# Kernel optimization log

Hardware: AMD Instinct MI355X
Metric: run time of the kernel (lower is better)

## Reference

```python
import jax, jax.numpy as jnp
import numpy as np
import math

B, S, D, H = 2, 2048, 1024, 16
DK = D // H


def setup_inputs() -> dict:
    key = jax.random.key(0)
    ks = jax.random.split(key, 12)
    std = 1.0 / math.sqrt(D)
    inp = {
        "q": jax.random.normal(ks[0], (B, S, D), jnp.float32),
        "k": jax.random.normal(ks[1], (B, S, D), jnp.float32),
        "v": jax.random.normal(ks[2], (B, S, D), jnp.float32),
        # causal mask, broadcast over batch and heads
        "mask": jnp.tril(jnp.ones((S, S), jnp.int32))[None, None, :, :],
        "wq": jax.random.normal(ks[3], (D, D), jnp.float32) * std,
        "bq": jax.random.normal(ks[4], (D,), jnp.float32) * std,
        "wk": jax.random.normal(ks[5], (D, D), jnp.float32) * std,
        "bk": jax.random.normal(ks[6], (D,), jnp.float32) * std,
        "wv": jax.random.normal(ks[7], (D, D), jnp.float32) * std,
        "bv": jax.random.normal(ks[8], (D,), jnp.float32) * std,
        "wo": jax.random.normal(ks[9], (D, D), jnp.float32) * std,
        "bo": jax.random.normal(ks[10], (D,), jnp.float32) * std,
    }
    return inp


def _split_heads(x):
    # [B,S,D] -> [B,H,S,DK]
    b, s, _ = x.shape
    return x.reshape(b, s, H, DK).transpose(0, 2, 1, 3)


def reference(q, k, v, mask, wq, bq, wk, bk, wv, bv, wo, bo):
    # nn.Linear: y = x @ W^T + b
    query = _split_heads(q @ wq.T + bq)
    key_h = _split_heads(k @ wk.T + bk)
    value = _split_heads(v @ wv.T + bv)

    scale = 1.0 / math.sqrt(DK)
    scores = jnp.einsum("bhqd,bhkd->bhqk", query, key_h) * scale  # [B,H,S,S]
    scores = jnp.where(mask == 0, jnp.float32(-1e9), scores)
    attn = jax.nn.softmax(scores, axis=-1)  # dropout p=0.0 -> identity

    x = jnp.einsum("bhqk,bhkd->bhqd", attn, value)  # [B,H,S,DK]
    x = x.transpose(0, 2, 1, 3).reshape(q.shape[0], -1, H * DK)  # [B,S,D]
    return x @ wo.T + bo
```

## Files before the change

### kernel.cpp

```cpp
#include <hip/hip_runtime.h>

#define B_SZ    2
#define S_LEN   2048
#define D_MODEL 1024
#define H_NUM   16
#define DK_H    64
#define M_ROWS  (B_SZ * S_LEN)

typedef __attribute__((ext_vector_type(8))) short  short8;
typedef __attribute__((ext_vector_type(4))) short  short4v;
typedef __attribute__((ext_vector_type(4))) float  floatx4;

__device__ __forceinline__ short f2b(float f) {
    union { float f; unsigned u; } x; x.f = f;
    unsigned u = x.u + 0x7fffu + ((x.u >> 16) & 1u);
    return (short)(u >> 16);
}

typedef __attribute__((address_space(1))) const unsigned int gu32;
typedef __attribute__((address_space(3))) unsigned int       lu32;
__device__ __forceinline__ void gload_lds16(const short* g, short* l) {
    __builtin_amdgcn_global_load_lds((gu32*)g, (lu32*)l, 16, 0, 0);
}

#define QSCALE 0.18033688011112042f
#define SM_SHIFT 12.0f

__global__ void cvt_all_kernel(const float* __restrict__ xq, const float* __restrict__ xk,
                               const float* __restrict__ xv, const float* __restrict__ wq,
                               const float* __restrict__ wk, const float* __restrict__ wv,
                               const float* __restrict__ wo,
                               short* __restrict__ oxq, short* __restrict__ oxk,
                               short* __restrict__ oxv, short* __restrict__ owq,
                               short* __restrict__ owk, short* __restrict__ owv,
                               short* __restrict__ owo)
{
    const int y = blockIdx.y;
    const float* in;
    short* out;
    switch (y) {
        case 0: in = xq; out = oxq; break;
        case 1: in = xk; out = oxk; break;
        case 2: in = xv; out = oxv; break;
        case 3: in = wq; out = owq; break;
        case 4: in = wk; out = owk; break;
        case 5: in = wv; out = owv; break;
        default: in = wo; out = owo; break;
    }
    if (y < 3) {
        int base = blockIdx.x * 1024 + threadIdx.x * 4;
        for (int p = 0; p < 4; ++p) {
            int i = base + p * 1048576;
            float4 v = *(const float4*)(in + i);
            short4v r;
            r[0] = f2b(v.x); r[1] = f2b(v.y); r[2] = f2b(v.z); r[3] = f2b(v.w);
            *(short4v*)(out + i) = r;
        }
    } else {
        int f = blockIdx.x * 256 + (int)threadIdx.x;
        if (blockIdx.x < 512) {
            int n4 = f >> 11, rem = f & 2047;
            int k8 = rem >> 4, nl = rem & 15;
            const float* src = in + (size_t)(n4 * 16 + nl) * D_MODEL + k8 * 8;
            float4 v0 = *(const float4*)(src);
            float4 v1 = *(const float4*)(src + 4);
            short8 r;
            r[0] = f2b(v0.x); r[1] = f2b(v0.y); r[2] = f2b(v0.z); r[3] = f2b(v0.w);
            r[4] = f2b(v1.x); r[5] = f2b(v1.y); r[6] = f2b(v1.z); r[7] = f2b(v1.w);
            *(short8*)(out + (size_t)f * 8) = r;
        }
    }
}

__global__ __launch_bounds__(256, 2)
void gemm_qkv_kernel(const short* __restrict__ xq, const short* __restrict__ xk,
                     const short* __restrict__ xv,
                     const short* __restrict__ wq, const short* __restrict__ wk,
                     const short* __restrict__ wv,
                     const float* __restrict__ bq, const float* __restrict__ bk,
                     const float* __restrict__ bv,
                     short* __restrict__ Qp, short* __restrict__ Kp, short* __restrict__ Vt)
{
    __shared__ short sa[128 * 32];

    const int which = blockIdx.y >> 3;
    const short* A    = (which == 0) ? xq : (which == 1) ? xk : xv;
    const short* W    = (which == 0) ? wq : (which == 1) ? wk : wv;
    const float* bias = (which == 0) ? bq : (which == 1) ? bk : bv;
    const float scale = (which == 0) ? QSCALE : 1.0f;

    const int nb = (blockIdx.y & 7) * 128;
    const int m0 = blockIdx.x * 128;
    const int t = threadIdx.x, wave = t >> 6, lane = t & 63;
    const int quad = lane >> 4, l16 = lane & 15;
    const int wm = (wave & 1) * 64, wn = (wave >> 1) * 64;

    const int r0 = t >> 2, cs = t & 3;
    const int c0 = cs ^ ((r0 >> 1) & 3);
    const short* Ab0 = A + (size_t)(m0 + r0) * D_MODEL + c0 * 8;
    const short* Ab1 = Ab0 + (size_t)64 * D_MODEL;
    short* sa0 = sa + t * 8;  short* sa1 = sa + 2048 + t * 8;

    int a_off[4];
#pragma unroll
    for (int i = 0; i < 4; ++i) {
        int ar = wm + i * 16 + l16;
        a_off[i] = ar * 32 + ((quad ^ ((ar >> 1) & 3)) * 8);
    }

    const short* Wt = W + ((size_t)((nb + wn) >> 4) * 128 + quad) * 128 + l16 * 8;

#define LOADB(dst, k0) do { _Pragma("unroll")                                  \
    for (int nt_ = 0; nt_ < 4; ++nt_)                                          \
        dst[nt_] = *(const short8*)(Wt + nt_ * 16384 + (k0) * 16); } while (0)

    short8 bfA[4], bfB[4];
    LOADB(bfA, 0);

    floatx4 acc[4][4] = {};
#pragma unroll 1
    for (int k0 = 0; k0 < D_MODEL; k0 += 64) {
        __syncthreads();
        gload_lds16(Ab0 + k0, sa0);
        gload_lds16(Ab1 + k0, sa1);
        __syncthreads();
        LOADB(bfB, k0 + 32);
#pragma unroll
        for (int mt = 0; mt < 4; ++mt) {
            short8 af = *(const short8*)(sa + a_off[mt]);
#pragma unroll
            for (int nt = 0; nt < 4; ++nt)
                acc[mt][nt] = __builtin_amdgcn_mfma_f32_16x16x32_bf16(af, bfA[nt], acc[mt][nt], 0, 0, 0);
        }
        __syncthreads();
        gload_lds16(Ab0 + k0 + 32, sa0);
        gload_lds16(Ab1 + k0 + 32, sa1);
        __syncthreads();
        if (k0 + 64 < D_MODEL) LOADB(bfA, k0 + 64);
#pragma unroll
        for (int mt = 0; mt < 4; ++mt) {
            short8 af = *(const short8*)(sa + a_off[mt]);
#pragma unroll
            for (int nt = 0; nt < 4; ++nt)
                acc[mt][nt] = __builtin_amdgcn_mfma_f32_16x16x32_bf16(af, bfB[nt], acc[mt][nt], 0, 0, 0);
        }
    }
#undef LOADB

#pragma unroll
    for (int nt = 0; nt < 4; ++nt) {
        int ncol = nb + wn + nt * 16 + l16;
        int h = ncol >> 6, dk = ncol & 63;
        float bv_ = bias[ncol];
#pragma unroll
        for (int mt = 0; mt < 4; ++mt) {
            int mrow0 = m0 + wm + mt * 16 + quad * 4;
            int bb = mrow0 >> 11, s0 = mrow0 & (S_LEN - 1);
            if (which < 2) {
                short* Out = (which == 0) ? Qp : Kp;
#pragma unroll
                for (int r = 0; r < 4; ++r) {
                    float v = (acc[mt][nt][r] + bv_) * scale;
                    Out[(((size_t)bb * H_NUM + h) * S_LEN + (s0 + r)) * DK_H + dk] = f2b(v);
                }
            } else {
                int Sb = s0 & ~63, sb0_ = s0 & 63;
                size_t rowbase = (((size_t)bb * H_NUM + h) * DK_H + dk) * S_LEN + Sb;
#pragma unroll
                for (int r = 0; r < 4; ++r) {
                    int cc = sb0_ + r;
                    Vt[rowbase + ((cc & 15) * 4 + (cc >> 4))] = f2b(acc[mt][nt][r] + bv_);
                }
            }
        }
    }
}

__global__ __launch_bounds__(512, 4)
void attn_kernel(const short* __restrict__ Qp, const short* __restrict__ Kp,
                 const short* __restrict__ Vt, short* __restrict__ Xa)
{
    __shared__ short kbuf[2][64 * 64];
    __shared__ short vbuf[2][64 * 64];
    __shared__ short pl[8][16 * 72];

    const int lin = (int)(blockIdx.x + 16 * blockIdx.y);
    const int bh = lin & 31;
    const int j8 = (lin >> 5) & 7;
    const int tile = (lin >> 8) ? (15 - j8) : j8;

    const int t = threadIdx.x, wave = t >> 6, lane = t & 63;
    const int quad = lane >> 4, l16 = lane & 15;

    const short* Qb  = Qp + (size_t)bh * S_LEN * DK_H;
    const short* Kb  = Kp + (size_t)bh * S_LEN * DK_H;
    const short* Vtb = Vt + (size_t)bh * DK_H * S_LEN;

    const int q0 = tile * 128 + wave * 16;
    const int my_ktimax = 2 * tile + (wave >> 2);
    const int ktb = 2 * tile + 1;

    const int r0 = t >> 3, cs = t & 7;
    const int c0 = cs ^ (r0 & 7);
    const short* Kg = Kb + r0 * DK_H + c0 * 8;
    const short* Vg = Vtb + (size_t)r0 * S_LEN + c0 * 8;
    short* kl0 = &kbuf[0][t * 8]; short* kl1 = &kbuf[1][t * 8];
    short* vl0 = &vbuf[0][t * 8]; short* vl1 = &vbuf[1][t * 8];

    short8 qf[2];
#pragma unroll
    for (int ks = 0; ks < 2; ++ks)
        qf[ks] = *(const short8*)(Qb + (size_t)(q0 + l16) * DK_H + ks * 32 + quad * 8);

    short8 bl = {};
    if (l16 == 0) {
#pragma unroll
        for (int j = 0; j < 8; ++j) bl[j] = (short)0x3F80;
    }

    int fo[4][2];
#pragma unroll
    for (int nt = 0; nt < 4; ++nt)
#pragma unroll
        for (int ks = 0; ks < 2; ++ks) {
            int row = nt * 16 + l16;
            fo[nt][ks] = row * 64 + (((ks * 4 + quad) ^ (l16 & 7)) * 8);
        }

    floatx4 o[4] = {};
    floatx4 ol = {};
    short* plw = &pl[wave][0];
    const int qg = q0 + quad * 4;

    gload_lds16(Kg, kl0);
    gload_lds16(Vg, vl0);
    __syncthreads();

    for (int kti = 0; kti <= ktb; ++kti) {
        const short* kb = (kti & 1) ? &kbuf[1][0] : &kbuf[0][0];
        const short* vb = (kti & 1) ? &vbuf[1][0] : &vbuf[0][0];
        const int kbase = kti * 64;

        if (kti < ktb) {
            gload_lds16(Kg + (size_t)(kbase + 64) * DK_H, (kti & 1) ? kl0 : kl1);
            gload_lds16(Vg + (kbase + 64),                (kti & 1) ? vl0 : vl1);
        }

        if (kti <= my_ktimax) {
            short8 bkf[4][2];
#pragma unroll
            for (int nt = 0; nt < 4; ++nt)
#pragma unroll
                for (int ks = 0; ks < 2; ++ks)
                    bkf[nt][ks] = *(const short8*)(kb + fo[nt][ks]);

            floatx4 sc[4] = {};
#pragma unroll
            for (int nt = 0; nt < 4; ++nt)
#pragma unroll
                for (int ks = 0; ks < 2; ++ks)
                    sc[nt] = __builtin_amdgcn_mfma_f32_16x16x32_bf16(qf[ks], bkf[nt][ks], sc[nt], 0, 0, 0);

            if (kti == my_ktimax) {
#pragma unroll
                for (int nt = 0; nt < 4; ++nt) {
                    int key = kbase + nt * 16 + l16;
#pragma unroll
                    for (int r = 0; r < 4; ++r)
                        if (key > qg + r) sc[nt][r] = -1e30f;
                }
            }

#pragma unroll
            for (int r = 0; r < 4; ++r) {
                union { float f; unsigned u; } a0, a1, a2, a3;
                a0.f = exp2f(sc[0][r] - SM_SHIFT);
                a1.f = exp2f(sc[1][r] - SM_SHIFT);
                a2.f = exp2f(sc[2][r] - SM_SHIFT);
                a3.f = exp2f(sc[3][r] - SM_SHIFT);
                uint2 d;
                d.x = (a1.u & 0xffff0000u) | (a0.u >> 16);
                d.y = (a3.u & 0xffff0000u) | (a2.u >> 16);
                *(uint2*)(plw + (quad * 4 + r) * 72 + l16 * 4) = d;
            }

            short8 ap0 = *(const short8*)(plw + l16 * 72 + quad * 8);
            short8 ap1 = *(const short8*)(plw + l16 * 72 + 32 + quad * 8);

            short8 bvf[4][2];
#pragma unroll
            for (int nt = 0; nt < 4; ++nt)
#pragma unroll
                for (int ks = 0; ks < 2; ++ks)
                    bvf[nt][ks] = *(const short8*)(vb + fo[nt][ks]);

#pragma unroll
            for (int nt = 0; nt < 4; ++nt) {
                o[nt] = __builtin_amdgcn_mfma_f32_16x16x32_bf16(ap0, bvf[nt][0], o[nt], 0, 0, 0);
                o[nt] = __builtin_amdgcn_mfma_f32_16x16x32_bf16(ap1, bvf[nt][1], o[nt], 0, 0, 0);
            }
            ol = __builtin_amdgcn_mfma_f32_16x16x32_bf16(ap0, bl, ol, 0, 0, 0);
            ol = __builtin_amdgcn_mfma_f32_16x16x32_bf16(ap1, bl, ol, 0, 0, 0);
        }

        __syncthreads();
    }

    const int b_ = bh >> 4, h = bh & 15;
#pragma unroll
    for (int r = 0; r < 4; ++r) {
        float lsum = __shfl(ol[r], (lane & 48));
        float rinv = 1.0f / lsum;
        int srow = qg + r;
#pragma unroll
        for (int nt = 0; nt < 4; ++nt) {
            int col = h * 64 + nt * 16 + l16;
            Xa[((size_t)b_ * S_LEN + srow) * D_MODEL + col] = f2b(o[nt][r] * rinv);
        }
    }
}

__global__ __launch_bounds__(256, 2)
void gemm_out_kernel(const short* __restrict__ A, const short* __restrict__ W,
                     const float* __restrict__ bias, float* __restrict__ out)
{
    __shared__ short sa[2][128 * 64];

    const int nb = blockIdx.y * 64;
    const int m0 = blockIdx.x * 128;
    const int t = threadIdx.x, wave = t >> 6, lane = t & 63;
    const int quad = lane >> 4, l16 = lane & 15;
    const int wm = (wave & 1) * 64, wn = (wave >> 1) * 32;

    const int rs = t >> 3;
    const int cl = (t & 7) ^ (rs & 7);
    const short* Asrc = A + (size_t)(m0 + rs) * D_MODEL + cl * 8;
    short* sd0 = &sa[0][t * 8];
    short* sd1 = &sa[1][t * 8];

#define STAGE_A(dst, k0) do { _Pragma("unroll")                                \
    for (int j_ = 0; j_ < 4; ++j_)                                             \
        gload_lds16(Asrc + (size_t)j_ * 32 * D_MODEL + (k0),                   \
                    (dst) + j_ * 2048); } while (0)

    int a_off[4][2];
#pragma unroll
    for (int i = 0; i < 4; ++i) {
        int ar = wm + i * 16 + l16;
#pragma unroll
        for (int ks = 0; ks < 2; ++ks)
            a_off[i][ks] = ar * 64 + (((ks * 4 + quad) ^ (ar & 7)) * 8);
    }

    const short* Wt = W + ((size_t)((nb + wn) >> 4) * 128 + quad) * 128 + l16 * 8;

#define LOADB2(dst, k0) do { _Pragma("unroll")                                 \
    for (int nt_ = 0; nt_ < 2; ++nt_)                                          \
        dst[nt_] = *(const short8*)(Wt + nt_ * 16384 + (k0) * 16); } while (0)

    short8 bfA[2], bfB[2];
    STAGE_A(sd0, 0);
    LOADB2(bfA, 0);
    __syncthreads();

    floatx4 acc[4][2] = {};
#pragma unroll 1
    for (int k0 = 0; k0 < D_MODEL; k0 += 64) {
        const int p = (k0 >> 6) & 1;
        const short* cur = &sa[p][0];
        if (k0 + 64 < D_MODEL) STAGE_A(p ? sd0 : sd1, k0 + 64);
        LOADB2(bfB, k0 + 32);

        short8 af[4][2];
#pragma unroll
        for (int mt = 0; mt < 4; ++mt) {
            af[mt][0] = *(const short8*)(cur + a_off[mt][0]);
            af[mt][1] = *(const short8*)(cur + a_off[mt][1]);
        }
#pragma unroll
        for (int mt = 0; mt < 4; ++mt)
#pragma unroll
            for (int nt = 0; nt < 2; ++nt)
                acc[mt][nt] = __builtin_amdgcn_mfma_f32_16x16x32_bf16(af[mt][0], bfA[nt], acc[mt][nt], 0, 0, 0);
        if (k0 + 64 < D_MODEL) LOADB2(bfA, k0 + 64);
#pragma unroll
        for (int mt = 0; mt < 4; ++mt)
#pragma unroll
            for (int nt = 0; nt < 2; ++nt)
                acc[mt][nt] = __builtin_amdgcn_mfma_f32_16x16x32_bf16(af[mt][1], bfB[nt], acc[mt][nt], 0, 0, 0);
        __syncthreads();
    }
#undef STAGE_A
#undef LOADB2

#pragma unroll
    for (int nt = 0; nt < 2; ++nt) {
        int ncol = nb + wn + nt * 16 + l16;
        float bv_ = bias[ncol];
#pragma unroll
        for (int mt = 0; mt < 4; ++mt) {
            int mrow0 = m0 + wm + mt * 16 + quad * 4;
#pragma unroll
            for (int r = 0; r < 4; ++r)
                out[(size_t)(mrow0 + r) * D_MODEL + ncol] = acc[mt][nt][r] + bv_;
        }
    }
}

extern "C" void kernel_launch(void* const* d_in, const int* in_sizes, int n_in,
                              void* d_out, int out_size, void* d_ws, size_t ws_size,
                              hipStream_t stream)
{
    (void)in_sizes; (void)n_in; (void)out_size; (void)ws_size;
    const float* q  = (const float*)d_in[0];
    const float* k  = (const float*)d_in[1];
    const float* v  = (const float*)d_in[2];
    const float* wq = (const float*)d_in[4];
    const float* bq = (const float*)d_in[5];
    const float* wk = (const float*)d_in[6];
    const float* bk = (const float*)d_in[7];
    const float* wv = (const float*)d_in[8];
    const float* bv = (const float*)d_in[9];
    const float* wo = (const float*)d_in[10];
    const float* bo = (const float*)d_in[11];
    float* out = (float*)d_out;

    const size_t XE = (size_t)M_ROWS * D_MODEL;
    const size_t WE = (size_t)D_MODEL * D_MODEL;
    short* ws_  = (short*)d_ws;
    short* xq_b = ws_;
    short* xk_b = xq_b + XE;
    short* xv_b = xk_b + XE;
    short* wq_b = xv_b + XE;
    short* wk_b = wq_b + WE;
    short* wv_b = wk_b + WE;
    short* wo_b = wv_b + WE;
    short* Qp   = wo_b + WE;
    short* Kp   = Qp + XE;
    short* Vt   = Kp + XE;
    short* Xa   = xq_b;

    dim3 blk(256);
    cvt_all_kernel<<<dim3(1024, 7), blk, 0, stream>>>(
        q, k, v, wq, wk, wv, wo, xq_b, xk_b, xv_b, wq_b, wk_b, wv_b, wo_b);

    gemm_qkv_kernel<<<dim3(M_ROWS / 128, 24), blk, 0, stream>>>(
        xq_b, xk_b, xv_b, wq_b, wk_b, wv_b, bq, bk, bv, Qp, Kp, Vt);

    attn_kernel<<<dim3(16, B_SZ * H_NUM), dim3(512), 0, stream>>>(Qp, Kp, Vt, Xa);

    gemm_out_kernel<<<dim3(M_ROWS / 128, D_MODEL / 64), blk, 0, stream>>>(Xa, wo_b, bo, out);
}
```

Before: 221.1 us.

## Process two 16-row query slices per wave in attention with 256-thread blocks

```diff
diff --git a/kernel.cpp b/kernel.cpp
--- a/kernel.cpp
+++ b/kernel.cpp
@@ -176,13 +176,13 @@
     }
 }
 
-__global__ __launch_bounds__(512, 4)
+__global__ __launch_bounds__(256, 2)
 void attn_kernel(const short* __restrict__ Qp, const short* __restrict__ Kp,
                  const short* __restrict__ Vt, short* __restrict__ Xa)
 {
     __shared__ short kbuf[2][64 * 64];
     __shared__ short vbuf[2][64 * 64];
-    __shared__ short pl[8][16 * 72];
+    __shared__ short pl[4][16 * 72];
 
     const int lin = (int)(blockIdx.x + 16 * blockIdx.y);
     const int bh = lin & 31;
@@ -196,8 +196,8 @@
     const short* Kb  = Kp + (size_t)bh * S_LEN * DK_H;
     const short* Vtb = Vt + (size_t)bh * DK_H * S_LEN;
 
-    const int q0 = tile * 128 + wave * 16;
-    const int my_ktimax = 2 * tile + (wave >> 2);
+    const int q0 = tile * 128 + wave * 32;
+    const int my_ktimax = 2 * tile + (wave >> 1);
     const int ktb = 2 * tile + 1;
 
     const int r0 = t >> 3, cs = t & 7;
@@ -207,10 +207,19 @@
     short* kl0 = &kbuf[0][t * 8]; short* kl1 = &kbuf[1][t * 8];
     short* vl0 = &vbuf[0][t * 8]; short* vl1 = &vbuf[1][t * 8];
 
-    short8 qf[2];
-#pragma unroll
-    for (int ks = 0; ks < 2; ++ks)
-        qf[ks] = *(const short8*)(Qb + (size_t)(q0 + l16) * DK_H + ks * 32 + quad * 8);
+#define STAGE_KV(kb_, vb_, kbase_) do {                                        \
+    gload_lds16(Kg + (size_t)(kbase_) * DK_H,            (kb_));               \
+    gload_lds16(Kg + (size_t)((kbase_) + 32) * DK_H,     (kb_) + 2048);        \
+    gload_lds16(Vg + (kbase_),                           (vb_));               \
+    gload_lds16(Vg + (kbase_) + 32 * S_LEN,              (vb_) + 2048);        \
+} while (0)
+
+    short8 qf[2][2];
+#pragma unroll
+    for (int h = 0; h < 2; ++h)
+#pragma unroll
+        for (int ks = 0; ks < 2; ++ks)
+            qf[h][ks] = *(const short8*)(Qb + (size_t)(q0 + h * 16 + l16) * DK_H + ks * 32 + quad * 8);
 
     short8 bl = {};
     if (l16 == 0) {
@@ -227,13 +236,12 @@
             fo[nt][ks] = row * 64 + (((ks * 4 + quad) ^ (l16 & 7)) * 8);
         }
 
-    floatx4 o[4] = {};
-    floatx4 ol = {};
+    floatx4 o[2][4] = {};
+    floatx4 ol[2] = {};
     short* plw = &pl[wave][0];
-    const int qg = q0 + quad * 4;
-
-    gload_lds16(Kg, kl0);
-    gload_lds16(Vg, vl0);
+    const int qgb = q0 + quad * 4;
+
+    STAGE_KV(kl0, vl0, 0);
     __syncthreads();
 
     for (int kti = 0; kti <= ktb; ++kti) {
@@ -242,8 +250,8 @@
         const int kbase = kti * 64;
 
         if (kti < ktb) {
-            gload_lds16(Kg + (size_t)(kbase + 64) * DK_H, (kti & 1) ? kl0 : kl1);
-            gload_lds16(Vg + (kbase + 64),                (kti & 1) ? vl0 : vl1);
+            if (kti & 1) STAGE_KV(kl0, vl0, kbase + 64);
+            else         STAGE_KV(kl1, vl1, kbase + 64);
         }
 
         if (kti <= my_ktimax) {
@@ -254,38 +262,27 @@
                 for (int ks = 0; ks < 2; ++ks)
                     bkf[nt][ks] = *(const short8*)(kb + fo[nt][ks]);
 
-            floatx4 sc[4] = {};
-#pragma unroll
-            for (int nt = 0; nt < 4; ++nt)
-#pragma unroll
-                for (int ks = 0; ks < 2; ++ks)
-                    sc[nt] = __builtin_amdgcn_mfma_f32_16x16x32_bf16(qf[ks], bkf[nt][ks], sc[nt], 0, 0, 0);
+            floatx4 sc[2][4] = {};
+#pragma unroll
+            for (int h = 0; h < 2; ++h)
+#pragma unroll
+                for (int nt = 0; nt < 4; ++nt)
+#pragma unroll
+                    for (int ks = 0; ks < 2; ++ks)
+                        sc[h][nt] = __builtin_amdgcn_mfma_f32_16x16x32_bf16(qf[h][ks], bkf[nt][ks], sc[h][nt], 0, 0, 0);
 
             if (kti == my_ktimax) {
 #pragma unroll
-                for (int nt = 0; nt < 4; ++nt) {
-                    int key = kbase + nt * 16 + l16;
-#pragma unroll
-                    for (int r = 0; r < 4; ++r)
-                        if (key > qg + r) sc[nt][r] = -1e30f;
-                }
+                for (int h = 0; h < 2; ++h)
+#pragma unroll
+                    for (int nt = 0; nt < 4; ++nt) {
+                        int key = kbase + nt * 16 + l16;
+                        int qg = qgb + h * 16;
+#pragma unroll
+                        for (int r = 0; r < 4; ++r)
+                            if (key > qg + r) sc[h][nt][r] = -1e30f;
+                    }
             }
-
-#pragma unroll
-            for (int r = 0; r < 4; ++r) {
-                union { float f; unsigned u; } a0, a1, a2, a3;
-                a0.f = exp2f(sc[0][r] - SM_SHIFT);
-                a1.f = exp2f(sc[1][r] - SM_SHIFT);
-                a2.f = exp2f(sc[2][r] - SM_SHIFT);
-                a3.f = exp2f(sc[3][r] - SM_SHIFT);
-                uint2 d;
-                d.x = (a1.u & 0xffff0000u) | (a0.u >> 16);
-                d.y = (a3.u & 0xffff0000u) | (a2.u >> 16);
-                *(uint2*)(plw + (quad * 4 + r) * 72 + l16 * 4) = d;
-            }
-
-            short8 ap0 = *(const short8*)(plw + l16 * 72 + quad * 8);
-            short8 ap1 = *(const short8*)(plw + l16 * 72 + 32 + quad * 8);
 
             short8 bvf[4][2];
 #pragma unroll
@@ -295,27 +292,49 @@
                     bvf[nt][ks] = *(const short8*)(vb + fo[nt][ks]);
 
 #pragma unroll
-            for (int nt = 0; nt < 4; ++nt) {
-                o[nt] = __builtin_amdgcn_mfma_f32_16x16x32_bf16(ap0, bvf[nt][0], o[nt], 0, 0, 0);
-                o[nt] = __builtin_amdgcn_mfma_f32_16x16x32_bf16(ap1, bvf[nt][1], o[nt], 0, 0, 0);
+            for (int h = 0; h < 2; ++h) {
+#pragma unroll
+                for (int r = 0; r < 4; ++r) {
+                    union { float f; unsigned u; } a0, a1, a2, a3;
+                    a0.f = exp2f(sc[h][0][r] - SM_SHIFT);
+                    a1.f = exp2f(sc[h][1][r] - SM_SHIFT);
+                    a2.f = exp2f(sc[h][2][r] - SM_SHIFT);
+                    a3.f = exp2f(sc[h][3][r] - SM_SHIFT);
+                    uint2 d;
+                    d.x = (a1.u & 0xffff0000u) | (a0.u >> 16);
+                    d.y = (a3.u & 0xffff0000u) | (a2.u >> 16);
+                    *(uint2*)(plw + (quad * 4 + r) * 72 + l16 * 4) = d;
+                }
+
+                short8 ap0 = *(const short8*)(plw + l16 * 72 + quad * 8);
+                short8 ap1 = *(const short8*)(plw + l16 * 72 + 32 + quad * 8);
+
+#pragma unroll
+                for (int nt = 0; nt < 4; ++nt) {
+                    o[h][nt] = __builtin_amdgcn_mfma_f32_16x16x32_bf16(ap0, bvf[nt][0], o[h][nt], 0, 0, 0);
+                    o[h][nt] = __builtin_amdgcn_mfma_f32_16x16x32_bf16(ap1, bvf[nt][1], o[h][nt], 0, 0, 0);
+                }
+                ol[h] = __builtin_amdgcn_mfma_f32_16x16x32_bf16(ap0, bl, ol[h], 0, 0, 0);
+                ol[h] = __builtin_amdgcn_mfma_f32_16x16x32_bf16(ap1, bl, ol[h], 0, 0, 0);
             }
-            ol = __builtin_amdgcn_mfma_f32_16x16x32_bf16(ap0, bl, ol, 0, 0, 0);
-            ol = __builtin_amdgcn_mfma_f32_16x16x32_bf16(ap1, bl, ol, 0, 0, 0);
-        }
-
-        __syncthreads();
-    }
-
-    const int b_ = bh >> 4, h = bh & 15;
+        }
+
+        __syncthreads();
+    }
+#undef STAGE_KV
+
+    const int b_ = bh >> 4, hh = bh & 15;
+#pragma unroll
+    for (int h = 0; h < 2; ++h)
 #pragma unroll
     for (int r = 0; r < 4; ++r) {
-        float lsum = __shfl(ol[r], (lane & 48));
+        float lsum = __shfl(ol[h][r], (lane & 48));
         float rinv = 1.0f / lsum;
-        int srow = qg + r;
+        int srow = qgb + h * 16 + r;
 #pragma unroll
         for (int nt = 0; nt < 4; ++nt) {
-            int col = h * 64 + nt * 16 + l16;
-            Xa[((size_t)b_ * S_LEN + srow) * D_MODEL + col] = f2b(o[nt][r] * rinv);
+            int col = hh * 64 + nt * 16 + l16;
+            Xa[((size_t)b_ * S_LEN + srow) * D_MODEL + col] = f2b(o[h][nt][r] * rinv);
         }
     }
 }
@@ -447,7 +466,7 @@
     gemm_qkv_kernel<<<dim3(M_ROWS / 128, 24), blk, 0, stream>>>(
         xq_b, xk_b, xv_b, wq_b, wk_b, wv_b, bq, bk, bv, Qp, Kp, Vt);
 
-    attn_kernel<<<dim3(16, B_SZ * H_NUM), dim3(512), 0, stream>>>(Qp, Kp, Vt, Xa);
+    attn_kernel<<<dim3(16, B_SZ * H_NUM), dim3(256), 0, stream>>>(Qp, Kp, Vt, Xa);
 
     gemm_out_kernel<<<dim3(M_ROWS / 128, D_MODEL / 64), blk, 0, stream>>>(Xa, wo_b, bo, out);
 }
```

Measured after the change: 238.9 us. +8.0%, slower.
